# Optimization experiments

Measured on AMD Instinct MI355X. Metric: run time of the kernel, lower is better.

The kernel has to match this reference:

```python
import jax, jax.numpy as jnp
import numpy as np

D = 768; H = 6; HD = D // H; DFF = 2048
L = 512; S = 1024; B = 8
EPS = 1e-5
SCALE = 1.0 / float(np.sqrt(2 * D // H))  # fused q/k head_dim = 2*D/H (Conditional-DETR attention)


def _ln(x, g, b):
    m = x.mean(-1, keepdims=True)
    v = ((x - m) ** 2).mean(-1, keepdims=True)
    return (x - m) / jnp.sqrt(v + EPS) * g + b


def _lin(x, w, b):  # w: (out, in) torch convention
    return jnp.einsum('lbd,ed->lbe', x, w) + b


def _fuse(c, p):  # channel-concat per head: (L,B,D)x2 -> (L,B,H,2*HD)
    Lx, Bx, _ = c.shape
    c = c.reshape(Lx, Bx, H, HD)
    p = p.reshape(Lx, Bx, H, HD)
    return jnp.concatenate([c, p], axis=-1)


def _attn(q, k, v, ow, ob):
    # q:(L,B,H,2HD) k:(S,B,H,2HD) v:(S,B,D); out_proj maps vdim->vdim
    Lx, Bx = q.shape[0], q.shape[1]
    Sx = k.shape[0]
    vh = v.reshape(Sx, Bx, H, HD)
    scores = jnp.einsum('lbhd,sbhd->bhls', q * SCALE, k)
    w = jax.nn.softmax(scores, axis=-1)
    o = jnp.einsum('bhls,sbhe->lbhe', w, vh).reshape(Lx, Bx, D)
    return _lin(o, ow, ob), w.mean(axis=1)  # head-averaged attn weights (B,L,S)


def setup_inputs() -> dict:
    key = jax.random.key(0)
    ks = iter(jax.random.split(key, 64))
    d = {}
    d['tgt'] = jax.random.normal(next(ks), (L, B, D), jnp.float32)
    d['memory'] = jax.random.normal(next(ks), (S, B, D), jnp.float32)
    d['tgt_pos'] = jax.random.normal(next(ks), (L, B, D), jnp.float32)
    d['memory_pos'] = jax.random.normal(next(ks), (S, B, D), jnp.float32)
    d['tgt_pos2'] = jax.random.normal(next(ks), (L, B, D), jnp.float32)

    def W(shape):
        return jax.random.normal(next(ks), shape, jnp.float32) * 0.02

    for pre in ('sa', 'ca'):
        for nm in ('qc', 'qp', 'kc', 'kp', 'v', 'o'):
            d[f'{pre}_{nm}_w'] = W((D, D))
            d[f'{pre}_{nm}_b'] = jnp.zeros((D,), jnp.float32)
    d['ff1_w'] = W((DFF, D)); d['ff1_b'] = jnp.zeros((DFF,), jnp.float32)
    d['ff2_w'] = W((D, DFF)); d['ff2_b'] = jnp.zeros((D,), jnp.float32)
    for i in (1, 2, 3):
        d[f'ln{i}_g'] = jnp.ones((D,), jnp.float32)
        d[f'ln{i}_b'] = jnp.zeros((D,), jnp.float32)
    return d


def reference(tgt, memory, tgt_pos, memory_pos, tgt_pos2,
              sa_qc_w, sa_qc_b, sa_qp_w, sa_qp_b, sa_kc_w, sa_kc_b, sa_kp_w, sa_kp_b,
              sa_v_w, sa_v_b, sa_o_w, sa_o_b,
              ca_qc_w, ca_qc_b, ca_qp_w, ca_qp_b, ca_kc_w, ca_kc_b, ca_kp_w, ca_kp_b,
              ca_v_w, ca_v_b, ca_o_w, ca_o_b,
              ff1_w, ff1_b, ff2_w, ff2_b,
              ln1_g, ln1_b, ln2_g, ln2_b, ln3_g, ln3_b):
    # --- self attention (dropout = identity at inference) ---
    q = _fuse(_lin(tgt_pos, sa_qc_w, sa_qc_b), _lin(tgt, sa_qp_w, sa_qp_b))
    k = _fuse(_lin(tgt_pos, sa_kc_w, sa_kc_b), _lin(tgt, sa_kp_w, sa_kp_b))
    v = _lin(tgt, sa_v_w, sa_v_b)
    t2, self_att = _attn(q, k, v, sa_o_w, sa_o_b)
    t = _ln(tgt + t2, ln1_g, ln1_b)
    # --- cross attention ---
    q = _fuse(_lin(tgt_pos, ca_qc_w, ca_qc_b), _lin(t + tgt_pos2, ca_qp_w, ca_qp_b))
    k = _fuse(_lin(memory, ca_kc_w, ca_kc_b), _lin(memory_pos, ca_kp_w, ca_kp_b))
    v = _lin(memory_pos, ca_v_w, ca_v_b)
    t2, att = _attn(q, k, v, ca_o_w, ca_o_b)
    t = _ln(t + t2, ln2_g, ln2_b)
    # --- FFN + post-norm ---
    t2 = _lin(jax.nn.relu(_lin(t, ff1_w, ff1_b)), ff2_w, ff2_b)
    t = _ln(t + t2, ln3_g, ln3_b)
    return (t, att, self_att)
```

## Files before the change

kernel.cpp:

```cpp
#include <hip/hip_runtime.h>


typedef __bf16 bf16;
typedef __attribute__((ext_vector_type(8))) __bf16 bf16x8;
typedef __attribute__((ext_vector_type(4))) float f32x4;

#define D_MODEL 768
#define NH 6
#define HD 128
#define ROWSTRIDE (8 * D_MODEL)

#define FENCE() asm volatile("" ::: "memory")

__device__ inline void swz_xyz(int& x, int& y, int& z) {
    const int nx = gridDim.x, ny = gridDim.y;
    const int n = nx * ny * gridDim.z;
    const int flat = blockIdx.x + nx * (blockIdx.y + ny * blockIdx.z);
    const int t = (flat & 7) * (n >> 3) + (flat >> 3);
    x = t % nx;
    const int r = t / nx;
    y = r % ny;
    z = r / ny;
}

__device__ __forceinline__ void gld16(const bf16* g, bf16* l) {
    __builtin_amdgcn_global_load_lds(
        (const __attribute__((address_space(1))) unsigned int*)g,
        (__attribute__((address_space(3))) unsigned int*)l, 16, 0, 0);
}

__device__ inline bf16x8 ld8f(const float* p) {
    f32x4 a = *(const f32x4*)p, b = *(const f32x4*)(p + 4);
    bf16x8 r;
#pragma unroll
    for (int i = 0; i < 4; i++) { r[i] = (bf16)a[i]; r[i + 4] = (bf16)b[i]; }
    return r;
}
__device__ inline bf16x8 ld8bf(const bf16* p, const float* q) {
    bf16x8 x = *(const bf16x8*)p;
    f32x4 a = *(const f32x4*)q, b = *(const f32x4*)(q + 4);
    bf16x8 r;
#pragma unroll
    for (int i = 0; i < 4; i++) { r[i] = (bf16)((float)x[i] + a[i]); r[i + 4] = (bf16)((float)x[i + 4] + b[i]); }
    return r;
}
__device__ inline bf16x8 ld8ff(const float* p, const float* q) {
    f32x4 a = *(const f32x4*)p, b = *(const f32x4*)(p + 4);
    f32x4 c = *(const f32x4*)q, d = *(const f32x4*)(q + 4);
    bf16x8 r;
#pragma unroll
    for (int i = 0; i < 4; i++) { r[i] = (bf16)(a[i] + c[i]); r[i + 4] = (bf16)(b[i] + d[i]); }
    return r;
}

struct CvtJob { const float* src; const float* src2; const bf16* add; bf16* dst; int nvec; };
struct CvtJobs { CvtJob j[12]; };

__global__ __launch_bounds__(256) void cvt_multi(CvtJobs jobs)
{
    const CvtJob jb = jobs.j[blockIdx.y];
    const int stride = gridDim.x * 256;
    if (jb.src2) {
        for (int i = blockIdx.x * 256 + threadIdx.x; i < jb.nvec; i += stride)
            *(bf16x8*)(jb.dst + (size_t)i * 8) = ld8ff(jb.src + (size_t)i * 8, jb.src2 + (size_t)i * 8);
    } else if (jb.add) {
        for (int i = blockIdx.x * 256 + threadIdx.x; i < jb.nvec; i += stride)
            *(bf16x8*)(jb.dst + (size_t)i * 8) = ld8bf(jb.add + (size_t)i * 8, jb.src + (size_t)i * 8);
    } else {
        for (int i = blockIdx.x * 256 + threadIdx.x; i < jb.nvec; i += stride)
            *(bf16x8*)(jb.dst + (size_t)i * 8) = ld8f(jb.src + (size_t)i * 8);
    }
}

struct JobM { const bf16* A; const bf16* W; const float* bias; bf16* C;
              int relu; int ycum; };
struct JobsM { JobM j[5]; };

__global__ __launch_bounds__(256) void gemm_multi(
    JobsM jobs, int lda, int ldw, int ldc, int K)
{
    __shared__ __align__(16) bf16 As[2][128 * 32];
    __shared__ __align__(16) bf16 Bs[2][128 * 32];
    int bx, byg, bzu;
    swz_xyz(bx, byg, bzu);
    int ji = 0;
    while (ji < 4 && byg >= jobs.j[ji].ycum) ji++;
    const JobM jb = jobs.j[ji];
    const int ybase = (ji == 0) ? 0 : jobs.j[ji - 1].ycum;
    const int bm = (byg - ybase) * 128, bn = bx * 128;
    const int tid = threadIdx.x;
    const int wave = tid >> 6, lane = tid & 63;
    const int wm = (wave >> 1) * 64, wn = (wave & 1) * 64;
    const int quad = lane >> 4, m16 = lane & 15;
    const int crow = lane >> 2, ccol = (lane & 3) * 8;
    const bf16* a0 = jb.A + (size_t)(bm + wave * 32 + crow) * lda + ccol;
    const bf16* a1 = a0 + (size_t)16 * lda;
    const bf16* w0 = jb.W + (size_t)(bn + wave * 32 + crow) * ldw + ccol;
    const bf16* w1 = w0 + (size_t)16 * ldw;
    const int wo = wave * 1024;
    f32x4 acc[4][4] = {};
    auto stage = [&](int buf, int k) {
        bf16* dA = As[buf] + wo;
        bf16* dB = Bs[buf] + wo;
        gld16(a0 + k, dA);
        gld16(a1 + k, dA + 512);
        gld16(w0 + k, dB);
        gld16(w1 + k, dB + 512);
    };
    auto compute = [&](int buf) {
        const bf16* rA = As[buf];
        const bf16* rB = Bs[buf];
        bf16x8 af[4], bfr[4];
#pragma unroll
        for (int i = 0; i < 4; i++) {
            af[i]  = *(const bf16x8*)&rA[(wm + i * 16 + m16) * 32 + quad * 8];
            bfr[i] = *(const bf16x8*)&rB[(wn + i * 16 + m16) * 32 + quad * 8];
        }
#pragma unroll
        for (int i = 0; i < 4; i++)
#pragma unroll
            for (int j = 0; j < 4; j++)
                acc[i][j] = __builtin_amdgcn_mfma_f32_16x16x32_bf16(af[i], bfr[j], acc[i][j], 0, 0, 0);
    };
    stage(0, 0);
    stage(1, 32);
    int cur = 0;
    for (int k0 = 0; k0 < K - 32; k0 += 32) {
        asm volatile("s_waitcnt vmcnt(4)" ::: "memory");
        __builtin_amdgcn_s_barrier();
        FENCE();
        compute(cur);
        FENCE();
        __builtin_amdgcn_s_barrier();
        FENCE();
        const int kp2 = k0 + 64;
        if (kp2 < K) stage(cur, kp2);
        cur ^= 1;
    }
    asm volatile("s_waitcnt vmcnt(0)" ::: "memory");
    __builtin_amdgcn_s_barrier();
    FENCE();
    compute(cur);
#pragma unroll
    for (int j = 0; j < 4; j++) {
        const int col = bn + wn + j * 16 + m16;
        const float bv = jb.bias[col];
#pragma unroll
        for (int i = 0; i < 4; i++)
#pragma unroll
            for (int r = 0; r < 4; r++) {
                const int row = bm + wm + i * 16 + quad * 4 + r;
                float val = acc[i][j][r] + bv;
                if (jb.relu) val = fmaxf(val, 0.f);
                jb.C[(size_t)row * ldc + col] = (bf16)val;
            }
    }
}

__global__ __launch_bounds__(256) void gemm_sk_bb(
    const bf16* __restrict__ A, int lda, const bf16* __restrict__ W, int ldw,
    float* __restrict__ Cp, size_t cstride, int ldc, int Ks)
{
    __shared__ __align__(16) bf16 As[2][128 * 32];
    __shared__ __align__(16) bf16 Bs[2][128 * 32];
    int bx, by, bz;
    swz_xyz(bx, by, bz);
    const int bm = by * 128, bn = bx * 128;
    const int kbase = bz * Ks;
    const int tid = threadIdx.x;
    const int wave = tid >> 6, lane = tid & 63;
    const int wm = (wave >> 1) * 64, wn = (wave & 1) * 64;
    const int quad = lane >> 4, m16 = lane & 15;
    const int crow = lane >> 2, ccol = (lane & 3) * 8;
    const bf16* a0 = A + (size_t)(bm + wave * 32 + crow) * lda + kbase + ccol;
    const bf16* a1 = a0 + (size_t)16 * lda;
    const bf16* w0 = W + (size_t)(bn + wave * 32 + crow) * ldw + kbase + ccol;
    const bf16* w1 = w0 + (size_t)16 * ldw;
    const int wo = wave * 1024;
    f32x4 acc[4][4] = {};
    auto stage = [&](int buf, int k) {
        bf16* dA = As[buf] + wo;
        bf16* dB = Bs[buf] + wo;
        gld16(a0 + k, dA);
        gld16(a1 + k, dA + 512);
        gld16(w0 + k, dB);
        gld16(w1 + k, dB + 512);
    };
    auto compute = [&](int buf) {
        const bf16* rA = As[buf];
        const bf16* rB = Bs[buf];
        bf16x8 af[4], bfr[4];
#pragma unroll
        for (int i = 0; i < 4; i++) {
            af[i]  = *(const bf16x8*)&rA[(wm + i * 16 + m16) * 32 + quad * 8];
            bfr[i] = *(const bf16x8*)&rB[(wn + i * 16 + m16) * 32 + quad * 8];
        }
#pragma unroll
        for (int i = 0; i < 4; i++)
#pragma unroll
            for (int j = 0; j < 4; j++)
                acc[i][j] = __builtin_amdgcn_mfma_f32_16x16x32_bf16(af[i], bfr[j], acc[i][j], 0, 0, 0);
    };
    stage(0, 0);
    stage(1, 32);
    int cur = 0;
    for (int k0 = 0; k0 < Ks - 32; k0 += 32) {
        asm volatile("s_waitcnt vmcnt(4)" ::: "memory");
        __builtin_amdgcn_s_barrier();
        FENCE();
        compute(cur);
        FENCE();
        __builtin_amdgcn_s_barrier();
        FENCE();
        const int kp2 = k0 + 64;
        if (kp2 < Ks) stage(cur, kp2);
        cur ^= 1;
    }
    asm volatile("s_waitcnt vmcnt(0)" ::: "memory");
    __builtin_amdgcn_s_barrier();
    FENCE();
    compute(cur);
    float* out = Cp + (size_t)bz * cstride;
#pragma unroll
    for (int j = 0; j < 4; j++) {
        const int col = bn + wn + j * 16 + m16;
#pragma unroll
        for (int i = 0; i < 4; i++)
#pragma unroll
            for (int r = 0; r < 4; r++) {
                const int row = bm + wm + i * 16 + quad * 4 + r;
                out[(size_t)row * ldc + col] = acc[i][j][r];
            }
    }
}

__global__ __launch_bounds__(256) void attn_scores(
    const bf16* __restrict__ qc, const bf16* __restrict__ qp,
    const bf16* __restrict__ kc, const bf16* __restrict__ kp,
    bf16* __restrict__ scores, int Lq, int S, float scale)
{
    __shared__ __align__(16) bf16 As[2][128 * 32];
    __shared__ __align__(16) bf16 Bs[2][128 * 32];
    int bx, by, bz;
    swz_xyz(bx, by, bz);
    const int bh = bz;
    const int b = bh / NH, h = bh % NH;
    const int bm = by * 128, bn = bx * 128;
    const int tid = threadIdx.x;
    const int wave = tid >> 6, lane = tid & 63;
    const int wm = (wave >> 1) * 64, wn = (wave & 1) * 64;
    const int quad = lane >> 4, m16 = lane & 15;
    const int crow = lane >> 2, ccol = (lane & 3) * 8;
    const size_t hb = (size_t)b * D_MODEL + h * HD;
    const size_t ar0 = (size_t)(bm + wave * 32 + crow) * ROWSTRIDE + hb + ccol;
    const size_t ar1 = ar0 + (size_t)16 * ROWSTRIDE;
    const size_t br0 = (size_t)(bn + wave * 32 + crow) * ROWSTRIDE + hb + ccol;
    const size_t br1 = br0 + (size_t)16 * ROWSTRIDE;
    const int wo = wave * 1024;
    f32x4 acc[4][4] = {};
    auto stage = [&](int buf, int k) {
        const bf16* qsrc = (k < 128) ? qc : qp;
        const bf16* ksrc = (k < 128) ? kc : kp;
        const int kcol = k & 127;
        bf16* dA = As[buf] + wo;
        bf16* dB = Bs[buf] + wo;
        gld16(qsrc + ar0 + kcol, dA);
        gld16(qsrc + ar1 + kcol, dA + 512);
        gld16(ksrc + br0 + kcol, dB);
        gld16(ksrc + br1 + kcol, dB + 512);
    };
    auto compute = [&](int buf) {
        const bf16* rA = As[buf];
        const bf16* rB = Bs[buf];
        bf16x8 af[4], bfr[4];
#pragma unroll
        for (int i = 0; i < 4; i++) {
            af[i]  = *(const bf16x8*)&rA[(wm + i * 16 + m16) * 32 + quad * 8];
            bfr[i] = *(const bf16x8*)&rB[(wn + i * 16 + m16) * 32 + quad * 8];
        }
#pragma unroll
        for (int i = 0; i < 4; i++)
#pragma unroll
            for (int j = 0; j < 4; j++)
                acc[i][j] = __builtin_amdgcn_mfma_f32_16x16x32_bf16(af[i], bfr[j], acc[i][j], 0, 0, 0);
    };
    stage(0, 0);
    stage(1, 32);
    int cur = 0;
    for (int k0 = 0; k0 < 224; k0 += 32) {
        asm volatile("s_waitcnt vmcnt(4)" ::: "memory");
        __builtin_amdgcn_s_barrier();
        FENCE();
        compute(cur);
        FENCE();
        __builtin_amdgcn_s_barrier();
        FENCE();
        const int kp2 = k0 + 64;
        if (kp2 < 256) stage(cur, kp2);
        cur ^= 1;
    }
    asm volatile("s_waitcnt vmcnt(0)" ::: "memory");
    __builtin_amdgcn_s_barrier();
    FENCE();
    compute(cur);
    bf16* sb = scores + (size_t)bh * Lq * S;
#pragma unroll
    for (int i = 0; i < 4; i++)
#pragma unroll
        for (int j = 0; j < 4; j++)
#pragma unroll
            for (int r = 0; r < 4; r++)
                sb[(size_t)(bm + wm + i * 16 + quad * 4 + r) * S + bn + wn + j * 16 + m16]
                    = (bf16)(acc[i][j][r] * scale);
}

template <int N>
__global__ __launch_bounds__(256) void softmax_mean(
    bf16* __restrict__ scores, float* __restrict__ att, int Lq)
{
    const int S = N << 8;
    const int l = blockIdx.x, b = blockIdx.y;
    const int tid = threadIdx.x;
    __shared__ float red[4], red2[4];
    float macc[N];
#pragma unroll
    for (int i = 0; i < N; i++) macc[i] = 0.f;
    for (int h = 0; h < NH; h++) {
        bf16* p = scores + ((size_t)(b * NH + h) * Lq + l) * S;
        float vals[N];
        float mx = -1e30f;
#pragma unroll
        for (int i = 0; i < N; i++) { vals[i] = (float)p[tid + (i << 8)]; mx = fmaxf(mx, vals[i]); }
        for (int off = 32; off; off >>= 1) mx = fmaxf(mx, __shfl_xor(mx, off, 64));
        if ((tid & 63) == 0) red[tid >> 6] = mx;
        __syncthreads();
        mx = fmaxf(fmaxf(red[0], red[1]), fmaxf(red[2], red[3]));
        float sum = 0.f;
#pragma unroll
        for (int i = 0; i < N; i++) { vals[i] = __expf(vals[i] - mx); sum += vals[i]; }
        for (int off = 32; off; off >>= 1) sum += __shfl_xor(sum, off, 64);
        if ((tid & 63) == 0) red2[tid >> 6] = sum;
        __syncthreads();
        const float inv = 1.f / (red2[0] + red2[1] + red2[2] + red2[3]);
#pragma unroll
        for (int i = 0; i < N; i++) {
            const float w = vals[i] * inv;
            p[tid + (i << 8)] = (bf16)w;
            macc[i] += w;
        }
    }
    float* ao = att + ((size_t)b * Lq + l) * S;
#pragma unroll
    for (int i = 0; i < N; i++) ao[tid + (i << 8)] = macc[i] * (1.f / 6.f);
}

__global__ __launch_bounds__(256) void attn_pv_sk(
    const bf16* __restrict__ wsm, const bf16* __restrict__ v,
    float* __restrict__ Pv, size_t pstride, int Lq, int S)
{
    __shared__ __align__(16) bf16 As[128 * 32];
    __shared__ __align__(16) bf16 BsT[128][40];
    int bx, by, bz;
    swz_xyz(bx, by, bz);
    const int bh = bz;
    const int b = bh / NH, h = bh % NH;
    const int bm = bx * 128;
    const int kbase = by * (S >> 1);
    const int tid = threadIdx.x;
    const int wave = tid >> 6, lane = tid & 63;
    const int wm = (wave >> 1) * 64, wn = (wave & 1) * 64;
    const int quad = lane >> 4, m16 = lane & 15;
    const int crow = lane >> 2, ccol = (lane & 3) * 8;
    const int kk0 = tid >> 4, e0 = (tid & 15) * 8;
    f32x4 acc[4][4] = {};
    const bf16* wbase = wsm + (size_t)(bh * Lq + bm) * S + kbase;
    const size_t vb = (size_t)b * D_MODEL + h * HD;
    const bf16* a0 = wbase + (size_t)(wave * 32 + crow) * S + ccol;
    const bf16* a1 = a0 + (size_t)16 * S;
    bf16* lA = As + wave * 1024;
    bf16x8 v0, v1;
    v0 = *(const bf16x8*)(v + (size_t)(kbase + kk0) * ROWSTRIDE + vb + e0);
    v1 = *(const bf16x8*)(v + (size_t)(kbase + kk0 + 16) * ROWSTRIDE + vb + e0);
    for (int k0 = 0; k0 < (S >> 1); k0 += 32) {
        gld16(a0 + k0, lA);
        gld16(a1 + k0, lA + 512);
#pragma unroll
        for (int i = 0; i < 8; i++) { BsT[e0 + i][kk0] = v0[i]; BsT[e0 + i][kk0 + 16] = v1[i]; }
        __syncthreads();
        const int kn = k0 + 32;
        if (kn < (S >> 1)) {
            v0 = *(const bf16x8*)(v + (size_t)(kbase + kn + kk0) * ROWSTRIDE + vb + e0);
            v1 = *(const bf16x8*)(v + (size_t)(kbase + kn + kk0 + 16) * ROWSTRIDE + vb + e0);
        }
        bf16x8 af[4], bfr[4];
#pragma unroll
        for (int i = 0; i < 4; i++) {
            af[i]  = *(const bf16x8*)&As[(wm + i * 16 + m16) * 32 + quad * 8];
            bfr[i] = *(const bf16x8*)&BsT[wn + i * 16 + m16][quad * 8];
        }
#pragma unroll
        for (int i = 0; i < 4; i++)
#pragma unroll
            for (int j = 0; j < 4; j++)
                acc[i][j] = __builtin_amdgcn_mfma_f32_16x16x32_bf16(af[i], bfr[j], acc[i][j], 0, 0, 0);
        __syncthreads();
    }
    float* out = Pv + by * pstride;
#pragma unroll
    for (int i = 0; i < 4; i++)
#pragma unroll
        for (int j = 0; j < 4; j++)
#pragma unroll
            for (int r = 0; r < 4; r++)
                out[(size_t)(bm + wm + i * 16 + quad * 4 + r) * ROWSTRIDE + vb + wn + j * 16 + m16]
                    = acc[i][j][r];
}

template <int NP, typename TR, typename TO>
__global__ __launch_bounds__(256) void add_ln_p(
    const TR* __restrict__ resid, const float* __restrict__ P, size_t pstride,
    const float* __restrict__ xbias,
    const float* __restrict__ g, const float* __restrict__ be, TO* __restrict__ out)
{
    const size_t base = (size_t)blockIdx.x * D_MODEL;
    const int tid = threadIdx.x;
    float v[3];
#pragma unroll
    for (int i = 0; i < 3; i++) {
        const int c = tid + (i << 8);
        float x = xbias[c];
#pragma unroll
        for (int p = 0; p < NP; p++) x += P[p * pstride + base + c];
        v[i] = (float)resid[base + c] + x;
    }
    float s = v[0] + v[1] + v[2];
    float s2 = v[0] * v[0] + v[1] * v[1] + v[2] * v[2];
    for (int off = 32; off; off >>= 1) { s += __shfl_xor(s, off, 64); s2 += __shfl_xor(s2, off, 64); }
    __shared__ float rs[4], rs2[4];
    if ((tid & 63) == 0) { rs[tid >> 6] = s; rs2[tid >> 6] = s2; }
    __syncthreads();
    s = rs[0] + rs[1] + rs[2] + rs[3];
    s2 = rs2[0] + rs2[1] + rs2[2] + rs2[3];
    const float mean = s * (1.f / 768.f);
    const float var = s2 * (1.f / 768.f) - mean * mean;
    const float inv = rsqrtf(var + 1e-5f);
#pragma unroll
    for (int i = 0; i < 3; i++) {
        const int c = tid + (i << 8);
        out[base + c] = (TO)((v[i] - mean) * inv * g[c] + be[c]);
    }
}

extern "C" void kernel_launch(void* const* d_in, const int* in_sizes, int n_in,
                              void* d_out, int out_size, void* d_ws, size_t ws_size,
                              hipStream_t stream)
{
    const float* tgt        = (const float*)d_in[0];
    const float* memory     = (const float*)d_in[1];
    const float* tgt_pos    = (const float*)d_in[2];
    const float* memory_pos = (const float*)d_in[3];
    const float* tgt_pos2   = (const float*)d_in[4];
    const float *sa_w[6], *sa_b[6], *ca_w[6], *ca_b[6];
    for (int i = 0; i < 6; i++) {
        sa_w[i] = (const float*)d_in[5 + 2 * i];  sa_b[i] = (const float*)d_in[6 + 2 * i];
        ca_w[i] = (const float*)d_in[17 + 2 * i]; ca_b[i] = (const float*)d_in[18 + 2 * i];
    }
    const float* ff1_w = (const float*)d_in[29]; const float* ff1_b = (const float*)d_in[30];
    const float* ff2_w = (const float*)d_in[31]; const float* ff2_b = (const float*)d_in[32];
    const float* ln_g[3] = {(const float*)d_in[33], (const float*)d_in[35], (const float*)d_in[37]};
    const float* ln_b[3] = {(const float*)d_in[34], (const float*)d_in[36], (const float*)d_in[38]};

    char* ws = (char*)d_ws;
    bf16* qc  = (bf16*)(ws);
    bf16* qp  = (bf16*)(ws + 6291456);
    bf16* kc  = (bf16*)(ws + 12582912);
    bf16* kp  = (bf16*)(ws + 25165824);
    bf16* vv  = (bf16*)(ws + 37748736);
    bf16* t1  = (bf16*)(ws + 50331648);
    bf16* sc  = (bf16*)(ws + 56623104);
    const size_t PSTRIDE = 3145728;
    float* pv_sa = (float*)(ws + 81788928);
    float* pv_ca = (float*)(ws + 12582912);
    float* op    = (float*)(ws + 56623104);
    float* fp    = (float*)(ws + 56623104);
    bf16*  tca   = kc;
    bf16*  ffh   = kp;

    bf16* tgt_b    = sc;
    bf16* mem_b    = sc;
    bf16* mempos_b = sc + 6291456;
    bf16* wb       = (bf16*)d_out;
    const size_t WSTEP = 589824;
    bf16* tp_b   = (bf16*)((char*)d_out + 12582912);
    bf16* qpin_b = tp_b + 3145728;
    bf16* ff1b   = qc;
    bf16* ff2b   = qp;
    bf16* savA   = kc;
    bf16* saw5b  = kc + 3145728;
    bf16* cavA   = vv;
    bf16* caw5b  = vv + 3145728;

    float* out_t    = (float*)d_out;
    float* out_att  = out_t + 3145728;
    float* out_satt = out_att + 4194304;

    const dim3 blk(256);
    const float SCALE = 0.0625f;
    const int BIG = 0x7fffffff;

    {
        CvtJobs C = {};
        for (int i = 0; i < 5; i++) C.j[i] = {sa_w[i], nullptr, nullptr, wb + i * WSTEP, 73728};
        for (int i = 0; i < 3; i++) C.j[5 + i] = {ca_w[2 + i], nullptr, nullptr, wb + (5 + i) * WSTEP, 73728};
        C.j[8]  = {ca_w[0], nullptr, nullptr, wb + 8 * WSTEP, 73728};
        C.j[9]  = {ca_w[1], nullptr, nullptr, wb + 9 * WSTEP, 73728};
        C.j[10] = {tgt,     nullptr, nullptr, tgt_b, 393216};
        C.j[11] = {tgt_pos, nullptr, nullptr, tp_b,  393216};
        cvt_multi<<<dim3(288, 12), blk, 0, stream>>>(C);
    }

    {
        JobsM J = {};
        J.j[0] = {tp_b,  wb + 0 * WSTEP, sa_b[0], qc, 0, 32};
        J.j[1] = {tgt_b, wb + 1 * WSTEP, sa_b[1], qp, 0, 64};
        J.j[2] = {tp_b,  wb + 2 * WSTEP, sa_b[2], kc, 0, 96};
        J.j[3] = {tgt_b, wb + 3 * WSTEP, sa_b[3], kp, 0, 128};
        J.j[4] = {tgt_b, wb + 4 * WSTEP, sa_b[4], vv, 0, 160};
        gemm_multi<<<dim3(6, 160), blk, 0, stream>>>(J, 768, 768, 768, 768);
    }
    attn_scores<<<dim3(4, 4, 48), blk, 0, stream>>>(qc, qp, kc, kp, sc, 512, 512, SCALE);
    softmax_mean<2><<<dim3(512, 8), blk, 0, stream>>>(sc, out_satt, 512);
    attn_pv_sk<<<dim3(4, 2, 48), blk, 0, stream>>>(sc, vv, pv_sa, PSTRIDE, 512, 512);
    {
        CvtJobs C = {};
        C.j[0] = {pv_sa, pv_sa + PSTRIDE, nullptr, savA,  393216};
        C.j[1] = {sa_w[5], nullptr,       nullptr, saw5b, 73728};
        cvt_multi<<<dim3(288, 2), blk, 0, stream>>>(C);
    }
    gemm_sk_bb<<<dim3(6, 32, 4), blk, 0, stream>>>(savA, 768, saw5b, 768,
                                                   op, PSTRIDE, 768, 192);
    add_ln_p<4, float, bf16><<<dim3(4096), blk, 0, stream>>>(tgt, op, PSTRIDE, sa_b[5],
                                                             ln_g[0], ln_b[0], t1);

    {
        CvtJobs C = {};
        C.j[0] = {memory,     nullptr, nullptr, mem_b,    786432};
        C.j[1] = {memory_pos, nullptr, nullptr, mempos_b, 786432};
        C.j[2] = {tgt_pos2,   nullptr, t1,      qpin_b,   393216};
        cvt_multi<<<dim3(288, 3), blk, 0, stream>>>(C);
    }

    {
        JobsM J = {};
        J.j[0] = {tp_b,     wb + 8 * WSTEP, ca_b[0], qc, 0, 32};
        J.j[1] = {qpin_b,   wb + 9 * WSTEP, ca_b[1], qp, 0, 64};
        J.j[2] = {mem_b,    wb + 5 * WSTEP, ca_b[2], kc, 0, 128};
        J.j[3] = {mempos_b, wb + 6 * WSTEP, ca_b[3], kp, 0, 192};
        J.j[4] = {mempos_b, wb + 7 * WSTEP, ca_b[4], vv, 0, 256};
        gemm_multi<<<dim3(6, 256), blk, 0, stream>>>(J, 768, 768, 768, 768);
    }
    attn_scores<<<dim3(8, 4, 48), blk, 0, stream>>>(qc, qp, kc, kp, sc, 512, 1024, SCALE);
    {
        CvtJobs C = {};
        C.j[0] = {ff1_w, nullptr, nullptr, ff1b, 196608};
        C.j[1] = {ff2_w, nullptr, nullptr, ff2b, 196608};
        cvt_multi<<<dim3(288, 2), blk, 0, stream>>>(C);
    }
    softmax_mean<4><<<dim3(512, 8), blk, 0, stream>>>(sc, out_att, 512);
    attn_pv_sk<<<dim3(4, 2, 48), blk, 0, stream>>>(sc, vv, pv_ca, PSTRIDE, 512, 1024);
    {
        CvtJobs C = {};
        C.j[0] = {pv_ca, pv_ca + PSTRIDE, nullptr, cavA,  393216};
        C.j[1] = {ca_w[5], nullptr,       nullptr, caw5b, 73728};
        cvt_multi<<<dim3(288, 2), blk, 0, stream>>>(C);
    }
    gemm_sk_bb<<<dim3(6, 32, 4), blk, 0, stream>>>(cavA, 768, caw5b, 768,
                                                   op, PSTRIDE, 768, 192);
    add_ln_p<4, bf16, bf16><<<dim3(4096), blk, 0, stream>>>(t1, op, PSTRIDE, ca_b[5],
                                                            ln_g[1], ln_b[1], tca);

    {
        JobsM J = {};
        J.j[0] = {tca, ff1b, ff1_b, ffh, 1, 32};
        J.j[1].ycum = BIG; J.j[2].ycum = BIG; J.j[3].ycum = BIG; J.j[4].ycum = BIG;
        gemm_multi<<<dim3(16, 32), blk, 0, stream>>>(J, 768, 768, 2048, 768);
    }
    gemm_sk_bb<<<dim3(6, 32, 4), blk, 0, stream>>>(ffh, 2048, ff2b, 2048,
                                                   fp, PSTRIDE, 768, 512);
    add_ln_p<4, bf16, float><<<dim3(4096), blk, 0, stream>>>(tca, fp, PSTRIDE, ff2_b,
                                                             ln_g[2], ln_b[2], out_t);
}
```

Before: 608.6 us.

## Fold fp32-to-bf16 conversions into softmax and layernorm kernels, halve out-proj split-K

The memory/memory_pos/qpin conversion pass is folded into a new fused add+LayerNorm kernel, and the FFN weight conversion is folded into the tail of the cross-attention softmax kernel. This removes two separate cvt launches and a re-read of t1. The output-projection split-K factor drops from 4 to 2, so the LayerNorm reads fewer partial sums in exchange for less K-parallelism per GEMM. To avoid aliasing with the scores buffer, mem_b and mempos_b move to another workspace region.

```diff
diff --git a/kernel.cpp b/kernel.cpp
--- a/kernel.cpp
+++ b/kernel.cpp
@@ -316,7 +316,8 @@
 
 template <int N>
 __global__ __launch_bounds__(256) void softmax_mean(
-    bf16* __restrict__ scores, float* __restrict__ att, int Lq)
+    bf16* __restrict__ scores, float* __restrict__ att, int Lq,
+    const float* cw1, bf16* cd1, int n1, const float* cw2, bf16* cd2, int n2)
 {
     const int S = N << 8;
     const int l = blockIdx.x, b = blockIdx.y;
@@ -352,6 +353,11 @@
     float* ao = att + ((size_t)b * Lq + l) * S;
 #pragma unroll
     for (int i = 0; i < N; i++) ao[tid + (i << 8)] = macc[i] * (1.f / 6.f);
+    if (cw1) {
+        const int gid = (blockIdx.y * gridDim.x + blockIdx.x) * 256 + tid;
+        if (gid < n1) *(bf16x8*)(cd1 + (size_t)gid * 8) = ld8f(cw1 + (size_t)gid * 8);
+        if (gid < n2) *(bf16x8*)(cd2 + (size_t)gid * 8) = ld8f(cw2 + (size_t)gid * 8);
+    }
 }
 
 __global__ __launch_bounds__(256) void attn_pv_sk(
@@ -451,6 +457,48 @@
     }
 }
 
+__global__ __launch_bounds__(256) void add_ln_fuse(
+    const float* __restrict__ resid, const float* __restrict__ P, size_t pstride,
+    const float* __restrict__ xbias,
+    const float* __restrict__ g, const float* __restrict__ be,
+    bf16* __restrict__ out, const float* __restrict__ tp2, bf16* __restrict__ qpin,
+    const float* __restrict__ mem, bf16* __restrict__ memb,
+    const float* __restrict__ mempos, bf16* __restrict__ memposb, int nmem)
+{
+    const size_t base = (size_t)blockIdx.x * D_MODEL;
+    const int tid = threadIdx.x;
+    float v[3];
+#pragma unroll
+    for (int i = 0; i < 3; i++) {
+        const int c = tid + (i << 8);
+        float x = xbias[c] + P[base + c] + P[pstride + base + c];
+        v[i] = resid[base + c] + x;
+    }
+    float s = v[0] + v[1] + v[2];
+    float s2 = v[0] * v[0] + v[1] * v[1] + v[2] * v[2];
+    for (int off = 32; off; off >>= 1) { s += __shfl_xor(s, off, 64); s2 += __shfl_xor(s2, off, 64); }
+    __shared__ float rs[4], rs2[4];
+    if ((tid & 63) == 0) { rs[tid >> 6] = s; rs2[tid >> 6] = s2; }
+    __syncthreads();
+    s = rs[0] + rs[1] + rs[2] + rs[3];
+    s2 = rs2[0] + rs2[1] + rs2[2] + rs2[3];
+    const float mean = s * (1.f / 768.f);
+    const float var = s2 * (1.f / 768.f) - mean * mean;
+    const float inv = rsqrtf(var + 1e-5f);
+#pragma unroll
+    for (int i = 0; i < 3; i++) {
+        const int c = tid + (i << 8);
+        const bf16 o = (bf16)((v[i] - mean) * inv * g[c] + be[c]);
+        out[base + c] = o;
+        qpin[base + c] = (bf16)((float)o + tp2[base + c]);
+    }
+    const int gid = blockIdx.x * 256 + tid;
+    if (gid < nmem) {
+        *(bf16x8*)(memb + (size_t)gid * 8) = ld8f(mem + (size_t)gid * 8);
+        *(bf16x8*)(memposb + (size_t)gid * 8) = ld8f(mempos + (size_t)gid * 8);
+    }
+}
+
 extern "C" void kernel_launch(void* const* d_in, const int* in_sizes, int n_in,
                               void* d_out, int out_size, void* d_ws, size_t ws_size,
                               hipStream_t stream)
@@ -487,8 +535,8 @@
     bf16*  ffh   = kp;
 
     bf16* tgt_b    = sc;
-    bf16* mem_b    = sc;
-    bf16* mempos_b = sc + 6291456;
+    bf16* mem_b    = (bf16*)(ws + 81788928);
+    bf16* mempos_b = mem_b + 6291456;
     bf16* wb       = (bf16*)d_out;
     const size_t WSTEP = 589824;
     bf16* tp_b   = (bf16*)((char*)d_out + 12582912);
@@ -529,7 +577,8 @@
         gemm_multi<<<dim3(6, 160), blk, 0, stream>>>(J, 768, 768, 768, 768);
     }
     attn_scores<<<dim3(4, 4, 48), blk, 0, stream>>>(qc, qp, kc, kp, sc, 512, 512, SCALE);
-    softmax_mean<2><<<dim3(512, 8), blk, 0, stream>>>(sc, out_satt, 512);
+    softmax_mean<2><<<dim3(512, 8), blk, 0, stream>>>(sc, out_satt, 512,
+                                                      nullptr, nullptr, 0, nullptr, nullptr, 0);
     attn_pv_sk<<<dim3(4, 2, 48), blk, 0, stream>>>(sc, vv, pv_sa, PSTRIDE, 512, 512);
     {
         CvtJobs C = {};
@@ -537,18 +586,12 @@
         C.j[1] = {sa_w[5], nullptr,       nullptr, saw5b, 73728};
         cvt_multi<<<dim3(288, 2), blk, 0, stream>>>(C);
     }
-    gemm_sk_bb<<<dim3(6, 32, 4), blk, 0, stream>>>(savA, 768, saw5b, 768,
-                                                   op, PSTRIDE, 768, 192);
-    add_ln_p<4, float, bf16><<<dim3(4096), blk, 0, stream>>>(tgt, op, PSTRIDE, sa_b[5],
-                                                             ln_g[0], ln_b[0], t1);
-
-    {
-        CvtJobs C = {};
-        C.j[0] = {memory,     nullptr, nullptr, mem_b,    786432};
-        C.j[1] = {memory_pos, nullptr, nullptr, mempos_b, 786432};
-        C.j[2] = {tgt_pos2,   nullptr, t1,      qpin_b,   393216};
-        cvt_multi<<<dim3(288, 3), blk, 0, stream>>>(C);
-    }
+    gemm_sk_bb<<<dim3(6, 32, 2), blk, 0, stream>>>(savA, 768, saw5b, 768,
+                                                   op, PSTRIDE, 768, 384);
+    add_ln_fuse<<<dim3(4096), blk, 0, stream>>>(tgt, op, PSTRIDE, sa_b[5],
+                                                ln_g[0], ln_b[0], t1,
+                                                tgt_pos2, qpin_b,
+                                                memory, mem_b, memory_pos, mempos_b, 786432);
 
     {
         JobsM J = {};
@@ -560,13 +603,9 @@
         gemm_multi<<<dim3(6, 256), blk, 0, stream>>>(J, 768, 768, 768, 768);
     }
     attn_scores<<<dim3(8, 4, 48), blk, 0, stream>>>(qc, qp, kc, kp, sc, 512, 1024, SCALE);
-    {
-        CvtJobs C = {};
-        C.j[0] = {ff1_w, nullptr, nullptr, ff1b, 196608};
-        C.j[1] = {ff2_w, nullptr, nullptr, ff2b, 196608};
-        cvt_multi<<<dim3(288, 2), blk, 0, stream>>>(C);
-    }
-    softmax_mean<4><<<dim3(512, 8), blk, 0, stream>>>(sc, out_att, 512);
+    softmax_mean<4><<<dim3(512, 8), blk, 0, stream>>>(sc, out_att, 512,
+                                                      ff1_w, ff1b, 196608,
+                                                      ff2_w, ff2b, 196608);
     attn_pv_sk<<<dim3(4, 2, 48), blk, 0, stream>>>(sc, vv, pv_ca, PSTRIDE, 512, 1024);
     {
         CvtJobs C = {};
@@ -574,9 +613,9 @@
         C.j[1] = {ca_w[5], nullptr,       nullptr, caw5b, 73728};
         cvt_multi<<<dim3(288, 2), blk, 0, stream>>>(C);
     }
-    gemm_sk_bb<<<dim3(6, 32, 4), blk, 0, stream>>>(cavA, 768, caw5b, 768,
-                                                   op, PSTRIDE, 768, 192);
-    add_ln_p<4, bf16, bf16><<<dim3(4096), blk, 0, stream>>>(t1, op, PSTRIDE, ca_b[5],
+    gemm_sk_bb<<<dim3(6, 32, 2), blk, 0, stream>>>(cavA, 768, caw5b, 768,
+                                                   op, PSTRIDE, 768, 384);
+    add_ln_p<2, bf16, bf16><<<dim3(4096), blk, 0, stream>>>(t1, op, PSTRIDE, ca_b[5],
                                                             ln_g[1], ln_b[1], tca);
 
     {
```

New measurement: 590.2 us. 1.03x faster.
